# Kernel optimization log

Measured on AMD Instinct MI355X. Metric: run time of the kernel, lower is better.

The kernel has to match this reference:

```python
import jax, jax.numpy as jnp
import numpy as np

N_XI = 512      # internal REN state dim
L = 128         # nonlinearity channels (sequential loop length)
N_STATES = 128  # plant state dim (w)
N_INPUTS = 64   # control input dim (u)
EPS = 0.001
STD = 0.1
BATCH = 32768


def _model_params(X, Y):
    """set_model_param(): derive constrained REN matrices from free params X, Y."""
    n, l = N_XI, L
    H = X.T @ X + EPS * jnp.eye(2 * n + l, dtype=X.dtype)
    H11 = H[:n, :n]
    H21 = H[n:n + l, :n]
    H22 = H[n:n + l, n:n + l]
    H31 = H[n + l:, :n]
    H32 = H[n + l:, n:n + l]
    H33 = H[n + l:, n + l:]
    Fm = H31                                 # (n_xi, n_xi)
    B1 = H32                                 # (n_xi, l)
    E = 0.5 * (H11 + H33 + Y - Y.T)          # (n_xi, n_xi)
    Lam = 0.5 * jnp.diag(H22)                # (l,) strictly positive
    D11 = -jnp.tril(H22, -1)                 # strictly lower triangular (l, l)
    C1 = -H21                                # (l, n_xi)
    return Fm, B1, E, Lam, D11, C1


def setup_inputs() -> dict:
    key = jax.random.key(0)
    ks = jax.random.split(key, 9)
    n, l = N_XI, L
    return {
        "t": 0,
        "w": jax.random.normal(ks[0], (BATCH, 1, N_STATES), jnp.float32),
        "xi": jax.random.normal(ks[1], (BATCH, 1, n), jnp.float32),
        "X": jax.random.normal(ks[2], (2 * n + l, 2 * n + l), jnp.float32) * STD,
        "Y": jax.random.normal(ks[3], (n, n), jnp.float32) * STD,
        "B2": jax.random.normal(ks[4], (n, N_STATES), jnp.float32) * STD,
        "C2": jax.random.normal(ks[5], (N_INPUTS, n), jnp.float32) * STD,
        "D21": jax.random.normal(ks[6], (N_INPUTS, l), jnp.float32) * STD,
        "D22": jax.random.normal(ks[7], (N_INPUTS, N_STATES), jnp.float32) * STD,
        "D12": jax.random.normal(ks[8], (l, N_STATES), jnp.float32) * STD,
    }


def reference(t, w, xi, X, Y, B2, C2, D21, D22, D12):
    Fm, B1, E, Lam, D11, C1 = _model_params(X, Y)
    w2 = w[:, 0, :]    # (B, num_states)
    xi2 = xi[:, 0, :]  # (B, n_xi)

    # Precompute the xi- and w-dependent parts of every row's pre-activation.
    pre = xi2 @ C1.T + w2 @ D12.T  # (B, l)

    eye = jnp.eye(L, dtype=pre.dtype)

    def step(eps, xs):
        # Sequential forward substitution: row i only reads eps[:, :i]
        # because D11 is strictly lower triangular.
        d_row, p_col, lam, e_row = xs
        v = p_col + eps @ d_row            # (B,)
        e = jnp.tanh(v / lam)
        return eps + e[:, None] * e_row[None, :], None

    eps0 = jnp.zeros_like(pre)
    epsilon, _ = jax.lax.scan(step, eps0, (D11, pre.T, Lam, eye))  # (B, l)

    E_xi = xi2 @ Fm.T + epsilon @ B1.T + w2 @ B2.T      # (B, n_xi)
    xi_ = E_xi @ jnp.linalg.inv(E).T                    # (B, n_xi)
    u = xi2 @ C2.T + epsilon @ D21.T + w2 @ D22.T       # (B, num_inputs)
    return u[:, None, :], xi_[:, None, :]
```

## Files before the change

kernel.cpp:

```cpp
#include <hip/hip_runtime.h>
#include <cstddef>

#define NXI   512
#define LL    128
#define NST   128
#define NU    64
#define BATCH 32768
#define TW    1152
#define EPSC  0.001f
#define KC    768
#define NC    576

typedef unsigned short u16;
typedef __attribute__((ext_vector_type(8))) short   short8;
typedef __attribute__((ext_vector_type(4))) short   short4v;
typedef __attribute__((ext_vector_type(4))) float   f32x4;

__device__ __forceinline__ u16 f2bf(float f) {
    unsigned u = __float_as_uint(f);
    u += 0x7FFFu + ((u >> 16) & 1u);
    return (u16)(u >> 16);
}

__global__ __launch_bounds__(256) void k_transpose(const float* __restrict__ X, u16* __restrict__ XT) {
    __shared__ float t[32][33];
    int tx = threadIdx.x & 31, ty = threadIdx.x >> 5;
    int bx = blockIdx.x, by = blockIdx.y;
    #pragma unroll
    for (int q = 0; q < 4; q++) {
        int r = ty + q * 8;
        t[r][tx] = X[(size_t)(by * 32 + r) * TW + bx * 32 + tx];
    }
    __syncthreads();
    #pragma unroll
    for (int q = 0; q < 4; q++) {
        int r = ty + q * 8;
        XT[(size_t)(bx * 32 + r) * TW + by * 32 + tx] = f2bf(t[tx][r]);
    }
}

__global__ __launch_bounds__(256) void k_build_Ac(const float* __restrict__ xi, const float* __restrict__ w,
                                                  u16* __restrict__ Ac) {
    size_t idx = ((size_t)blockIdx.x * 256 + threadIdx.x) * 8;
    int b = (int)(idx / KC), c = (int)(idx % KC);
    float v[8];
    if (c < 512) {
        const f32x4* s = (const f32x4*)(xi + (size_t)b * NXI + c);
        f32x4 a = s[0], bb = s[1];
        v[0]=a[0]; v[1]=a[1]; v[2]=a[2]; v[3]=a[3]; v[4]=bb[0]; v[5]=bb[1]; v[6]=bb[2]; v[7]=bb[3];
    } else if (c < 640) {
        #pragma unroll
        for (int j = 0; j < 8; j++) v[j] = 0.f;
    } else {
        const f32x4* s = (const f32x4*)(w + (size_t)b * NST + (c - 640));
        f32x4 a = s[0], bb = s[1];
        v[0]=a[0]; v[1]=a[1]; v[2]=a[2]; v[3]=a[3]; v[4]=bb[0]; v[5]=bb[1]; v[6]=bb[2]; v[7]=bb[3];
    }
    short8 o;
    #pragma unroll
    for (int j = 0; j < 8; j++) o[j] = (short)f2bf(v[j]);
    *(short8*)(Ac + idx) = o;
}

#define LDT 40
__global__ __launch_bounds__(256) void k_gemm(const u16* __restrict__ A, int lda,
                                              const u16* __restrict__ W, int ldw,
                                              float* __restrict__ C0, int ldc0, int nsplit,
                                              float* __restrict__ C1, int ldc1, int K) {
    __shared__ __align__(16) u16 As[128 * LDT];
    __shared__ __align__(16) u16 Bs[64 * LDT];
    int tid = threadIdx.x;
    int wave = tid >> 6, lane = tid & 63, quad = lane >> 4, l16 = lane & 15;
    int bm0 = blockIdx.y * 128, bn0 = blockIdx.x * 64;
    f32x4 acc[2][4];
    #pragma unroll
    for (int i = 0; i < 2; i++)
        #pragma unroll
        for (int j = 0; j < 4; j++) acc[i][j] = (f32x4){0.f, 0.f, 0.f, 0.f};

    int sr = tid >> 1, sh = tid & 1;
    for (int kt = 0; kt < K; kt += 32) {
        __syncthreads();
        {
            const f32x4* sa = (const f32x4*)(A + (size_t)(bm0 + sr) * lda + kt + sh * 16);
            f32x4 v0 = sa[0], v1 = sa[1];
            f32x4* da = (f32x4*)&As[sr * LDT + sh * 16];
            da[0] = v0; da[1] = v1;
            if (tid < 128) {
                int br = tid >> 1, bh = tid & 1;
                const f32x4* sb = (const f32x4*)(W + (size_t)(bn0 + br) * ldw + kt + bh * 16);
                f32x4 u0 = sb[0], u1 = sb[1];
                f32x4* db = (f32x4*)&Bs[br * LDT + bh * 16];
                db[0] = u0; db[1] = u1;
            }
        }
        __syncthreads();
        short8 af0 = *(const short8*)&As[(wave * 32 + l16) * LDT + quad * 8];
        short8 af1 = *(const short8*)&As[(wave * 32 + 16 + l16) * LDT + quad * 8];
        #pragma unroll
        for (int nt = 0; nt < 4; nt++) {
            short8 wf = *(const short8*)&Bs[(nt * 16 + l16) * LDT + quad * 8];
            acc[0][nt] = __builtin_amdgcn_mfma_f32_16x16x32_bf16(af0, wf, acc[0][nt], 0, 0, 0);
            acc[1][nt] = __builtin_amdgcn_mfma_f32_16x16x32_bf16(af1, wf, acc[1][nt], 0, 0, 0);
        }
    }
    #pragma unroll
    for (int mt = 0; mt < 2; mt++)
        #pragma unroll
        for (int nt = 0; nt < 4; nt++)
            #pragma unroll
            for (int r = 0; r < 4; r++) {
                int row = bm0 + wave * 32 + mt * 16 + quad * 4 + r;
                int col = bn0 + nt * 16 + l16;
                float v = acc[mt][nt][r];
                if (col < nsplit) C0[(size_t)row * ldc0 + col] = v;
                else              C1[(size_t)row * ldc1 + (col - nsplit)] = v;
            }
}

__global__ __launch_bounds__(256) void k_derive(const float* __restrict__ Hm, const float* __restrict__ Y,
                                                const float* __restrict__ B2, const float* __restrict__ D12,
                                                float* __restrict__ Agj, float* __restrict__ D11,
                                                float* __restrict__ rlam, u16* __restrict__ W1) {
    int idx = blockIdx.x * 256 + threadIdx.x;
    const int n0 = 512 * 1280, n1 = 128 * 128, n2 = 128, n3 = 128 * KC;
    if (idx < n0) {
        int i = idx / 1280, j = idx % 1280;
        float val;
        if (j < 512) {
            val = 0.5f * (Hm[(size_t)i * TW + j] + Hm[(size_t)(640 + i) * TW + 640 + j]
                          + Y[(size_t)i * 512 + j] - Y[(size_t)j * 512 + i]);
            if (i == j) val += EPSC;
        } else if (j < 1024) {
            val = Hm[(size_t)(640 + i) * TW + (j - 512)];
        } else if (j < 1152) {
            val = Hm[(size_t)(640 + i) * TW + 512 + (j - 1024)];
        } else {
            val = B2[(size_t)i * NST + (j - 1152)];
        }
        Agj[idx] = val;
        return;
    }
    idx -= n0;
    if (idx < n1) {
        int i = idx >> 7, j = idx & 127;
        D11[idx] = (j < i) ? -Hm[(size_t)(512 + i) * TW + 512 + j] : 0.f;
        return;
    }
    idx -= n1;
    if (idx < n2) {
        rlam[idx] = 2.0f / (Hm[(size_t)(512 + idx) * TW + 512 + idx] + EPSC);
        return;
    }
    idx -= n2;
    if (idx < n3) {
        int i = idx / KC, c = idx % KC;
        float v;
        if (c < 512)      v = -Hm[(size_t)(512 + i) * TW + c];
        else if (c < 640) v = 0.f;
        else              v = D12[(size_t)i * NST + (c - 640)];
        W1[(size_t)i * KC + c] = f2bf(v);
    }
}

__device__ __forceinline__ void invert64(float* Cl, float* Sa, float* Sb, float* mcol,
                                         float* rp, float* __restrict__ invOut, int tid) {
    int r = tid >> 2, c = tid & 3;
    float a[16], b[16];
    #pragma unroll
    for (int q = 0; q < 4; q++) {
        f32x4 v = *(f32x4*)&Cl[r * 68 + c * 16 + q * 4];
        a[q*4+0]=v[0]; a[q*4+1]=v[1]; a[q*4+2]=v[2]; a[q*4+3]=v[3];
    }
    #pragma unroll
    for (int j = 0; j < 16; j++) b[j] = (c * 16 + j == r) ? 1.f : 0.f;

    #pragma unroll
    for (int k = 0; k < 64; k++) {
        const int kc = k >> 4, kl = k & 15;
        if (r == k) {
            #pragma unroll
            for (int q = 0; q < 4; q++) {
                *(f32x4*)&Sa[c * 16 + q * 4] = (f32x4){a[q*4], a[q*4+1], a[q*4+2], a[q*4+3]};
                *(f32x4*)&Sb[c * 16 + q * 4] = (f32x4){b[q*4], b[q*4+1], b[q*4+2], b[q*4+3]};
            }
        }
        if (c == kc) {
            mcol[r] = a[kl];
            if (r == k) rp[0] = 1.0f / a[kl];
        }
        __syncthreads();
        float m = (mcol[r] - ((r == k) ? 1.0f : 0.0f)) * rp[0];
        #pragma unroll
        for (int q = 0; q < 4; q++) {
            f32x4 sa = *(f32x4*)&Sa[c * 16 + q * 4];
            f32x4 sb = *(f32x4*)&Sb[c * 16 + q * 4];
            a[q*4+0] = fmaf(-m, sa[0], a[q*4+0]); a[q*4+1] = fmaf(-m, sa[1], a[q*4+1]);
            a[q*4+2] = fmaf(-m, sa[2], a[q*4+2]); a[q*4+3] = fmaf(-m, sa[3], a[q*4+3]);
            b[q*4+0] = fmaf(-m, sb[0], b[q*4+0]); b[q*4+1] = fmaf(-m, sb[1], b[q*4+1]);
            b[q*4+2] = fmaf(-m, sb[2], b[q*4+2]); b[q*4+3] = fmaf(-m, sb[3], b[q*4+3]);
        }
        __syncthreads();
    }
    #pragma unroll
    for (int q = 0; q < 4; q++)
        *(f32x4*)&invOut[r * 64 + c * 16 + q * 4] = (f32x4){b[q*4], b[q*4+1], b[q*4+2], b[q*4+3]};
}

__global__ __launch_bounds__(256) void k_diaginv0(const float* __restrict__ Agj, float* __restrict__ invD) {
    __shared__ __align__(16) float Cl[64 * 68];
    __shared__ float Sa[64], Sb[64], mcol[64], rp[1];
    int tid = threadIdx.x, r = tid >> 2, c4 = tid & 3;
    #pragma unroll
    for (int q = 0; q < 4; q++)
        *(f32x4*)&Cl[r * 68 + c4 * 16 + q * 4] = *(const f32x4*)(Agj + (size_t)r * 1280 + c4 * 16 + q * 4);
    __syncthreads();
    invert64(Cl, Sa, Sb, mcol, rp, invD, tid);
}

__global__ __launch_bounds__(256) void k_elim(float* __restrict__ Agj, float* __restrict__ invD, int k) {
    __shared__ __align__(16) float invDs[64 * 68];
    __shared__ __align__(16) float Ps[64 * 68];
    __shared__ __align__(16) float Ss[64 * 68];
    __shared__ __align__(16) float Ms[64 * 68];
    __shared__ float Sa[64], Sb[64], mcol[64], rp[1];
    int tid = threadIdx.x;
    int by = blockIdx.y, bx = blockIdx.x;
    int rb = by + (by >= k ? 1 : 0);
    int cb = k + 1 + bx;
    int lr = tid >> 2, lc = tid & 3;
    #pragma unroll
    for (int q = 0; q < 4; q++) {
        *(f32x4*)&invDs[lr * 68 + lc * 16 + q * 4] = *(const f32x4*)(invD + (size_t)k * 4096 + lr * 64 + lc * 16 + q * 4);
        *(f32x4*)&Ps[lr * 68 + lc * 16 + q * 4]    = *(const f32x4*)(Agj + (size_t)(k * 64 + lr) * 1280 + cb * 64 + lc * 16 + q * 4);
        *(f32x4*)&Ms[lr * 68 + lc * 16 + q * 4]    = *(const f32x4*)(Agj + (size_t)(rb * 64 + lr) * 1280 + k * 64 + lc * 16 + q * 4);
    }
    __syncthreads();
    int ty = tid >> 4, tx = tid & 15;
    f32x4 s[4];
    #pragma unroll
    for (int ri = 0; ri < 4; ri++) s[ri] = (f32x4){0.f, 0.f, 0.f, 0.f};
    for (int kk = 0; kk < 64; kk++) {
        f32x4 pv = *(f32x4*)&Ps[kk * 68 + tx * 4];
        #pragma unroll
        for (int ri = 0; ri < 4; ri++) s[ri] += pv * invDs[(ty * 4 + ri) * 68 + kk];
    }
    #pragma unroll
    for (int ri = 0; ri < 4; ri++) *(f32x4*)&Ss[(ty * 4 + ri) * 68 + tx * 4] = s[ri];
    __syncthreads();
    f32x4 accv[4];
    #pragma unroll
    for (int ri = 0; ri < 4; ri++)
        accv[ri] = *(const f32x4*)(Agj + (size_t)(rb * 64 + ty * 4 + ri) * 1280 + cb * 64 + tx * 4);
    for (int kk = 0; kk < 64; kk++) {
        f32x4 sv = *(f32x4*)&Ss[kk * 68 + tx * 4];
        #pragma unroll
        for (int ri = 0; ri < 4; ri++) accv[ri] -= sv * Ms[(ty * 4 + ri) * 68 + kk];
    }
    #pragma unroll
    for (int ri = 0; ri < 4; ri++)
        *(f32x4*)(Agj + (size_t)(rb * 64 + ty * 4 + ri) * 1280 + cb * 64 + tx * 4) = accv[ri];
    if (k < 7 && bx == 0 && by == k) {
        __syncthreads();
        #pragma unroll
        for (int ri = 0; ri < 4; ri++) *(f32x4*)&Ps[(ty * 4 + ri) * 68 + tx * 4] = accv[ri];
        __syncthreads();
        invert64(Ps, Sa, Sb, mcol, rp, invD + (size_t)(k + 1) * 4096, tid);
    }
}

__global__ __launch_bounds__(256) void k_finalize(const float* __restrict__ Agj, const float* __restrict__ invD,
                                                  const float* __restrict__ C2, const float* __restrict__ D21,
                                                  const float* __restrict__ D22, u16* __restrict__ Wc) {
    __shared__ __align__(16) float invDs[64 * 68];
    __shared__ __align__(16) float Ps[64 * 68];
    int tid = threadIdx.x, bx = blockIdx.x, by = blockIdx.y;
    int ty = tid >> 4, tx = tid & 15;
    if (by == 8) {
        #pragma unroll
        for (int ri = 0; ri < 4; ri++) {
            int q = ty * 4 + ri;
            int cbase = bx * 64 + tx * 4;
            f32x4 v;
            if (cbase < 512)      v = *(const f32x4*)(C2 + (size_t)q * 512 + cbase);
            else if (cbase < 640) v = *(const f32x4*)(D21 + (size_t)q * NST + (cbase - 512));
            else                  v = *(const f32x4*)(D22 + (size_t)q * NST + (cbase - 640));
            short4v o; o[0]=(short)f2bf(v[0]); o[1]=(short)f2bf(v[1]); o[2]=(short)f2bf(v[2]); o[3]=(short)f2bf(v[3]);
            *(short4v*)(Wc + (size_t)(512 + q) * KC + cbase) = o;
        }
        return;
    }
    int lr = tid >> 2, lc = tid & 3;
    #pragma unroll
    for (int q = 0; q < 4; q++) {
        *(f32x4*)&invDs[lr * 68 + lc * 16 + q * 4] = *(const f32x4*)(invD + (size_t)by * 4096 + lr * 64 + lc * 16 + q * 4);
        *(f32x4*)&Ps[lr * 68 + lc * 16 + q * 4]    = *(const f32x4*)(Agj + (size_t)(by * 64 + lr) * 1280 + 512 + bx * 64 + lc * 16 + q * 4);
    }
    __syncthreads();
    f32x4 s[4];
    #pragma unroll
    for (int ri = 0; ri < 4; ri++) s[ri] = (f32x4){0.f, 0.f, 0.f, 0.f};
    for (int kk = 0; kk < 64; kk++) {
        f32x4 pv = *(f32x4*)&Ps[kk * 68 + tx * 4];
        #pragma unroll
        for (int ri = 0; ri < 4; ri++) s[ri] += pv * invDs[(ty * 4 + ri) * 68 + kk];
    }
    #pragma unroll
    for (int ri = 0; ri < 4; ri++) {
        short4v o; o[0]=(short)f2bf(s[ri][0]); o[1]=(short)f2bf(s[ri][1]); o[2]=(short)f2bf(s[ri][2]); o[3]=(short)f2bf(s[ri][3]);
        *(short4v*)(Wc + (size_t)(by * 64 + ty * 4 + ri) * KC + bx * 64 + tx * 4) = o;
    }
}

__global__ __launch_bounds__(1024) void k_scan(const float* __restrict__ pre, const float* __restrict__ D11,
                                               const float* __restrict__ rlam, u16* __restrict__ Ac) {
    __shared__ __align__(16) float D11s[128 * 132];
    int tid = threadIdx.x;
    {
        int r = tid >> 3, c = (tid & 7) * 16;
        const f32x4* src = (const f32x4*)(D11 + (size_t)r * 128 + c);
        f32x4 v0 = src[0], v1 = src[1], v2 = src[2], v3 = src[3];
        f32x4* dst = (f32x4*)&D11s[r * 132 + c];
        dst[0] = v0; dst[1] = v1; dst[2] = v2; dst[3] = v3;
    }
    int lg = tid & 15;
    int row = blockIdx.x * 64 + (tid >> 4);
    int gbase = (tid & 63) & ~15;
    const float L2E2 = 2.885390082f;

    float corrv[8], a8[8];
    #pragma unroll
    for (int b = 0; b < 8; b++) {
        corrv[b] = pre[(size_t)row * 128 + b * 16 + lg];
        a8[b] = L2E2 * rlam[b * 16 + lg];
    }
    __syncthreads();

    #pragma unroll
    for (int b = 0; b < 8; b++) {
        f32x4 dblk[4];
        #pragma unroll
        for (int q = 0; q < 4; q++)
            dblk[q] = *(const f32x4*)&D11s[(b * 16 + lg) * 132 + b * 16 + q * 4];
        float v = corrv[b];
        float a = a8[b];
        float e16[16];
        float myeps = 0.f;
        #pragma unroll
        for (int t = 0; t < 16; t++) {
            float ex = __builtin_amdgcn_exp2f(a * v);
            float cand = 1.0f - 2.0f * __builtin_amdgcn_rcpf(ex + 1.0f);
            float e = __shfl(cand, gbase + t, 64);
            e16[t] = e;
            if (lg == t) myeps = e;
            v = fmaf(e, dblk[t >> 2][t & 3], v);
        }
        Ac[(size_t)row * KC + 512 + b * 16 + lg] = f2bf(myeps);
        #pragma unroll
        for (int bb = b + 1; bb < 8; bb++) {
            f32x4 dd[4];
            #pragma unroll
            for (int q = 0; q < 4; q++)
                dd[q] = *(const f32x4*)&D11s[(bb * 16 + lg) * 132 + b * 16 + q * 4];
            float acc = corrv[bb];
            #pragma unroll
            for (int t = 0; t < 16; t++)
                acc = fmaf(e16[t], dd[t >> 2][t & 3], acc);
            corrv[bb] = acc;
        }
    }
}

extern "C" void kernel_launch(void* const* d_in, const int* in_sizes, int n_in,
                              void* d_out, int out_size, void* d_ws, size_t ws_size,
                              hipStream_t stream) {
    const float* w_in  = (const float*)d_in[1];
    const float* xi_in = (const float*)d_in[2];
    const float* X   = (const float*)d_in[3];
    const float* Y   = (const float*)d_in[4];
    const float* B2  = (const float*)d_in[5];
    const float* C2  = (const float*)d_in[6];
    const float* D21 = (const float*)d_in[7];
    const float* D22 = (const float*)d_in[8];
    const float* D12 = (const float*)d_in[9];
    float* out_u  = (float*)d_out;
    float* out_xi = (float*)d_out + (size_t)BATCH * NU;

    char* base = (char*)d_ws;
    size_t off = 0;
    auto carve = [&](size_t bytes) -> void* {
        void* p = base + off;
        off += (bytes + 255) & ~(size_t)255;
        return p;
    };
    u16*   XT   = (u16*)  carve((size_t)TW * TW * 2);
    u16*   Ac   = (u16*)  carve((size_t)BATCH * KC * 2);
    float* Hm   = (float*)carve((size_t)TW * TW * 4);
    float* Agj  = (float*)carve((size_t)512 * 1280 * 4);
    float* invD = (float*)carve((size_t)8 * 64 * 64 * 4);
    u16*   Wc   = (u16*)  carve((size_t)NC * KC * 2);
    u16*   W1   = (u16*)  carve((size_t)LL * KC * 2);
    float* pre  = (float*)carve((size_t)BATCH * LL * 4);
    float* D11  = (float*)carve((size_t)LL * LL * 4);
    float* rlam = (float*)carve((size_t)LL * 4);
    (void)ws_size; (void)in_sizes; (void)n_in; (void)out_size;

    k_transpose<<<dim3(36, 36), 256, 0, stream>>>(X, XT);
    k_build_Ac<<<(BATCH * KC / 8 + 255) / 256, 256, 0, stream>>>(xi_in, w_in, Ac);
    k_gemm<<<dim3(TW / 64, TW / 128), 256, 0, stream>>>(XT, TW, XT, TW, Hm, TW, 1 << 30, nullptr, 0, TW);
    k_derive<<<(512 * 1280 + 128 * 128 + 128 + 128 * KC + 255) / 256, 256, 0, stream>>>(
        Hm, Y, B2, D12, Agj, D11, rlam, W1);
    k_diaginv0<<<1, 256, 0, stream>>>(Agj, invD);
    for (int k = 0; k < 8; k++)
        k_elim<<<dim3(19 - k, 7), 256, 0, stream>>>(Agj, invD, k);
    k_finalize<<<dim3(12, 9), 256, 0, stream>>>(Agj, invD, C2, D21, D22, Wc);
    k_gemm<<<dim3(LL / 64, BATCH / 128), 256, 0, stream>>>(Ac, KC, W1, KC, pre, LL, 1 << 30, nullptr, 0, KC);
    k_scan<<<BATCH / 64, 1024, 0, stream>>>(pre, D11, rlam, Ac);
    k_gemm<<<dim3(NC / 64, BATCH / 128), 256, 0, stream>>>(Ac, KC, Wc, KC, out_xi, NXI, 512, out_u, NU, KC);
}
```

Before: 580.5 us.

## Replace GEMM with 128x128 tiles, direct global-to-LDS loads and swizzled block order

The bf16 GEMM kernel is replaced by one using 128x128 output tiles, each wave computing 64x64 with 4x4 MFMAs. Tiles are staged with global_load_lds direct copies, and blocks can be remapped in a swizzled order for L2 locality. The Wc weight is padded to 640 rows with zeros so the N dimension divides the tile, and stores are masked to the true width. k_build_Ac now writes only the xi and w chunks and skips the zero band. This raises data reuse per loaded byte and cuts load instructions, at the cost of higher register use and an unpadded LDS layout that may cause bank conflicts.

```diff
diff --git a/kernel.cpp b/kernel.cpp
--- a/kernel.cpp
+++ b/kernel.cpp
@@ -10,6 +10,7 @@
 #define EPSC  0.001f
 #define KC    768
 #define NC    576
+#define NCP   640
 
 typedef unsigned short u16;
 typedef __attribute__((ext_vector_type(8))) short   short8;
@@ -41,80 +42,86 @@
 
 __global__ __launch_bounds__(256) void k_build_Ac(const float* __restrict__ xi, const float* __restrict__ w,
                                                   u16* __restrict__ Ac) {
-    size_t idx = ((size_t)blockIdx.x * 256 + threadIdx.x) * 8;
-    int b = (int)(idx / KC), c = (int)(idx % KC);
-    float v[8];
-    if (c < 512) {
-        const f32x4* s = (const f32x4*)(xi + (size_t)b * NXI + c);
-        f32x4 a = s[0], bb = s[1];
-        v[0]=a[0]; v[1]=a[1]; v[2]=a[2]; v[3]=a[3]; v[4]=bb[0]; v[5]=bb[1]; v[6]=bb[2]; v[7]=bb[3];
-    } else if (c < 640) {
-        #pragma unroll
-        for (int j = 0; j < 8; j++) v[j] = 0.f;
+    size_t t = (size_t)blockIdx.x * 256 + threadIdx.x;
+    int b = (int)(t / 80), ch = (int)(t % 80);
+    const float* src;
+    int col;
+    if (ch < 64) { src = xi + (size_t)b * NXI + ch * 8;        col = ch * 8; }
+    else         { src = w  + (size_t)b * NST + (ch - 64) * 8; col = 640 + (ch - 64) * 8; }
+    f32x4 a = ((const f32x4*)src)[0], c = ((const f32x4*)src)[1];
+    short8 o;
+    o[0]=(short)f2bf(a[0]); o[1]=(short)f2bf(a[1]); o[2]=(short)f2bf(a[2]); o[3]=(short)f2bf(a[3]);
+    o[4]=(short)f2bf(c[0]); o[5]=(short)f2bf(c[1]); o[6]=(short)f2bf(c[2]); o[7]=(short)f2bf(c[3]);
+    *(short8*)(Ac + (size_t)b * KC + col) = o;
+}
+
+__global__ __launch_bounds__(256) void k_gemm2(const u16* __restrict__ A, int lda,
+                                               const u16* __restrict__ W, int ldw,
+                                               float* __restrict__ C0, int ldc0, int nsplit,
+                                               float* __restrict__ C1, int ldc1,
+                                               int K, int nbx, int ntrue, int swz) {
+    __shared__ __align__(16) u16 As[128 * 32];
+    __shared__ __align__(16) u16 Bs[128 * 32];
+    int id = blockIdx.x;
+    int bx, by;
+    if (swz) {
+        int j = id >> 3;
+        int per = (int)(gridDim.x >> 3) / nbx;
+        by = (id & 7) * per + j / nbx;
+        bx = j - (j / nbx) * nbx;
     } else {
-        const f32x4* s = (const f32x4*)(w + (size_t)b * NST + (c - 640));
-        f32x4 a = s[0], bb = s[1];
-        v[0]=a[0]; v[1]=a[1]; v[2]=a[2]; v[3]=a[3]; v[4]=bb[0]; v[5]=bb[1]; v[6]=bb[2]; v[7]=bb[3];
-    }
-    short8 o;
-    #pragma unroll
-    for (int j = 0; j < 8; j++) o[j] = (short)f2bf(v[j]);
-    *(short8*)(Ac + idx) = o;
-}
-
-#define LDT 40
-__global__ __launch_bounds__(256) void k_gemm(const u16* __restrict__ A, int lda,
-                                              const u16* __restrict__ W, int ldw,
-                                              float* __restrict__ C0, int ldc0, int nsplit,
-                                              float* __restrict__ C1, int ldc1, int K) {
-    __shared__ __align__(16) u16 As[128 * LDT];
-    __shared__ __align__(16) u16 Bs[64 * LDT];
-    int tid = threadIdx.x;
-    int wave = tid >> 6, lane = tid & 63, quad = lane >> 4, l16 = lane & 15;
-    int bm0 = blockIdx.y * 128, bn0 = blockIdx.x * 64;
-    f32x4 acc[2][4];
-    #pragma unroll
-    for (int i = 0; i < 2; i++)
+        by = id / nbx;
+        bx = id - by * nbx;
+    }
+    const int tid = threadIdx.x;
+    const int wave = tid >> 6, lane = tid & 63, quad = lane >> 4, l16 = lane & 15;
+    const int bm0 = by * 128, bn0 = bx * 128;
+    const int srow = tid >> 2, sch = (tid & 3) * 8;
+    const u16* ga0 = A + (size_t)(bm0 + srow) * lda + sch;
+    const u16* ga1 = ga0 + (size_t)64 * lda;
+    const u16* gb0 = W + (size_t)(bn0 + srow) * ldw + sch;
+    const u16* gb1 = gb0 + (size_t)64 * ldw;
+    u16* la = As + wave * 512;
+    u16* lb = Bs + wave * 512;
+    const int mb = (wave >> 1) * 64, nb = (wave & 1) * 64;
+
+    f32x4 acc[4][4];
+    #pragma unroll
+    for (int i = 0; i < 4; i++)
         #pragma unroll
         for (int j = 0; j < 4; j++) acc[i][j] = (f32x4){0.f, 0.f, 0.f, 0.f};
 
-    int sr = tid >> 1, sh = tid & 1;
     for (int kt = 0; kt < K; kt += 32) {
         __syncthreads();
-        {
-            const f32x4* sa = (const f32x4*)(A + (size_t)(bm0 + sr) * lda + kt + sh * 16);
-            f32x4 v0 = sa[0], v1 = sa[1];
-            f32x4* da = (f32x4*)&As[sr * LDT + sh * 16];
-            da[0] = v0; da[1] = v1;
-            if (tid < 128) {
-                int br = tid >> 1, bh = tid & 1;
-                const f32x4* sb = (const f32x4*)(W + (size_t)(bn0 + br) * ldw + kt + bh * 16);
-                f32x4 u0 = sb[0], u1 = sb[1];
-                f32x4* db = (f32x4*)&Bs[br * LDT + bh * 16];
-                db[0] = u0; db[1] = u1;
-            }
-        }
-        __syncthreads();
-        short8 af0 = *(const short8*)&As[(wave * 32 + l16) * LDT + quad * 8];
-        short8 af1 = *(const short8*)&As[(wave * 32 + 16 + l16) * LDT + quad * 8];
-        #pragma unroll
-        for (int nt = 0; nt < 4; nt++) {
-            short8 wf = *(const short8*)&Bs[(nt * 16 + l16) * LDT + quad * 8];
-            acc[0][nt] = __builtin_amdgcn_mfma_f32_16x16x32_bf16(af0, wf, acc[0][nt], 0, 0, 0);
-            acc[1][nt] = __builtin_amdgcn_mfma_f32_16x16x32_bf16(af1, wf, acc[1][nt], 0, 0, 0);
-        }
-    }
-    #pragma unroll
-    for (int mt = 0; mt < 2; mt++)
+        __builtin_amdgcn_global_load_lds((void*)(ga0 + kt), (void*)la,          16, 0, 0);
+        __builtin_amdgcn_global_load_lds((void*)(ga1 + kt), (void*)(la + 2048), 16, 0, 0);
+        __builtin_amdgcn_global_load_lds((void*)(gb0 + kt), (void*)lb,          16, 0, 0);
+        __builtin_amdgcn_global_load_lds((void*)(gb1 + kt), (void*)(lb + 2048), 16, 0, 0);
+        __syncthreads();
+        short8 af[4], bf[4];
+        #pragma unroll
+        for (int mt = 0; mt < 4; mt++) af[mt] = *(const short8*)&As[(mb + mt * 16 + l16) * 32 + quad * 8];
+        #pragma unroll
+        for (int nt = 0; nt < 4; nt++) bf[nt] = *(const short8*)&Bs[(nb + nt * 16 + l16) * 32 + quad * 8];
+        #pragma unroll
+        for (int mt = 0; mt < 4; mt++)
+            #pragma unroll
+            for (int nt = 0; nt < 4; nt++)
+                acc[mt][nt] = __builtin_amdgcn_mfma_f32_16x16x32_bf16(af[mt], bf[nt], acc[mt][nt], 0, 0, 0);
+    }
+    #pragma unroll
+    for (int mt = 0; mt < 4; mt++)
         #pragma unroll
         for (int nt = 0; nt < 4; nt++)
             #pragma unroll
             for (int r = 0; r < 4; r++) {
-                int row = bm0 + wave * 32 + mt * 16 + quad * 4 + r;
-                int col = bn0 + nt * 16 + l16;
-                float v = acc[mt][nt][r];
-                if (col < nsplit) C0[(size_t)row * ldc0 + col] = v;
-                else              C1[(size_t)row * ldc1 + (col - nsplit)] = v;
+                int row = bm0 + mb + mt * 16 + quad * 4 + r;
+                int col = bn0 + nb + nt * 16 + l16;
+                if (col < ntrue) {
+                    float v = acc[mt][nt][r];
+                    if (col < nsplit) C0[(size_t)row * ldc0 + col] = v;
+                    else              C1[(size_t)row * ldc1 + (col - nsplit)] = v;
+                }
             }
 }
 
@@ -276,17 +283,23 @@
     __shared__ __align__(16) float Ps[64 * 68];
     int tid = threadIdx.x, bx = blockIdx.x, by = blockIdx.y;
     int ty = tid >> 4, tx = tid & 15;
-    if (by == 8) {
+    if (by >= 8) {
         #pragma unroll
         for (int ri = 0; ri < 4; ri++) {
             int q = ty * 4 + ri;
+            int row = 512 + (by - 8) * 64 + q;
             int cbase = bx * 64 + tx * 4;
-            f32x4 v;
-            if (cbase < 512)      v = *(const f32x4*)(C2 + (size_t)q * 512 + cbase);
-            else if (cbase < 640) v = *(const f32x4*)(D21 + (size_t)q * NST + (cbase - 512));
-            else                  v = *(const f32x4*)(D22 + (size_t)q * NST + (cbase - 640));
-            short4v o; o[0]=(short)f2bf(v[0]); o[1]=(short)f2bf(v[1]); o[2]=(short)f2bf(v[2]); o[3]=(short)f2bf(v[3]);
-            *(short4v*)(Wc + (size_t)(512 + q) * KC + cbase) = o;
+            short4v o;
+            if (by == 8) {
+                f32x4 v;
+                if (cbase < 512)      v = *(const f32x4*)(C2 + (size_t)q * 512 + cbase);
+                else if (cbase < 640) v = *(const f32x4*)(D21 + (size_t)q * NST + (cbase - 512));
+                else                  v = *(const f32x4*)(D22 + (size_t)q * NST + (cbase - 640));
+                o[0]=(short)f2bf(v[0]); o[1]=(short)f2bf(v[1]); o[2]=(short)f2bf(v[2]); o[3]=(short)f2bf(v[3]);
+            } else {
+                o[0]=0; o[1]=0; o[2]=0; o[3]=0;
+            }
+            *(short4v*)(Wc + (size_t)row * KC + cbase) = o;
         }
         return;
     }
@@ -398,7 +411,7 @@
     float* Hm   = (float*)carve((size_t)TW * TW * 4);
     float* Agj  = (float*)carve((size_t)512 * 1280 * 4);
     float* invD = (float*)carve((size_t)8 * 64 * 64 * 4);
-    u16*   Wc   = (u16*)  carve((size_t)NC * KC * 2);
+    u16*   Wc   = (u16*)  carve((size_t)NCP * KC * 2);
     u16*   W1   = (u16*)  carve((size_t)LL * KC * 2);
     float* pre  = (float*)carve((size_t)BATCH * LL * 4);
     float* D11  = (float*)carve((size_t)LL * LL * 4);
@@ -406,15 +419,15 @@
     (void)ws_size; (void)in_sizes; (void)n_in; (void)out_size;
 
     k_transpose<<<dim3(36, 36), 256, 0, stream>>>(X, XT);
-    k_build_Ac<<<(BATCH * KC / 8 + 255) / 256, 256, 0, stream>>>(xi_in, w_in, Ac);
-    k_gemm<<<dim3(TW / 64, TW / 128), 256, 0, stream>>>(XT, TW, XT, TW, Hm, TW, 1 << 30, nullptr, 0, TW);
+    k_build_Ac<<<BATCH * 80 / 256, 256, 0, stream>>>(xi_in, w_in, Ac);
+    k_gemm2<<<81, 256, 0, stream>>>(XT, TW, XT, TW, Hm, TW, 1 << 30, nullptr, 0, TW, 9, TW, 0);
     k_derive<<<(512 * 1280 + 128 * 128 + 128 + 128 * KC + 255) / 256, 256, 0, stream>>>(
         Hm, Y, B2, D12, Agj, D11, rlam, W1);
     k_diaginv0<<<1, 256, 0, stream>>>(Agj, invD);
     for (int k = 0; k < 8; k++)
         k_elim<<<dim3(19 - k, 7), 256, 0, stream>>>(Agj, invD, k);
-    k_finalize<<<dim3(12, 9), 256, 0, stream>>>(Agj, invD, C2, D21, D22, Wc);
-    k_gemm<<<dim3(LL / 64, BATCH / 128), 256, 0, stream>>>(Ac, KC, W1, KC, pre, LL, 1 << 30, nullptr, 0, KC);
+    k_finalize<<<dim3(12, 10), 256, 0, stream>>>(Agj, invD, C2, D21, D22, Wc);
+    k_gemm2<<<256, 256, 0, stream>>>(Ac, KC, W1, KC, pre, LL, 1 << 30, nullptr, 0, KC, 1, LL, 1);
     k_scan<<<BATCH / 64, 1024, 0, stream>>>(pre, D11, rlam, Ac);
-    k_gemm<<<dim3(NC / 64, BATCH / 128), 256, 0, stream>>>(Ac, KC, Wc, KC, out_xi, NXI, 512, out_u, NU, KC);
-}
+    k_gemm2<<<1280, 256, 0, stream>>>(Ac, KC, Wc, KC, out_xi, NXI, 512, out_u, NU, KC, 5, NC, 1);
+}
```

New measurement: 528.2 us. 1.1x faster.
